# Optimization experiments

Measured on AMD Instinct MI355X. Metric: run time of the kernel, lower is better.

## Reference

```python
import jax, jax.numpy as jnp
import numpy as np

DEPTH = 4      # truncation depth of the signature
DIM = 8        # path channels
PATH_LEN = 16384
STREAM = True


def _restricted_exp(z, depth):
    # exp(z) in truncated tensor algebra: level k term = z^{\otimes k}/k!, flattened to [d**k]
    terms = [z]
    for k in range(2, depth + 1):
        terms.append((terms[-1][:, None] * z[None, :]).reshape(-1) / k)
    return tuple(terms)


def _chen_mult(a, b, depth):
    # Truncated tensor-algebra product (Chen's relation); a_0 = b_0 = 1 implicit.
    # c_k = a_k + b_k + sum_{i=1}^{k-1} a_i \otimes b_{k-i}
    c = []
    for k in range(depth):
        t = a[k] + b[k]
        for i in range(k):
            t = t + (a[i][:, None] * b[k - 1 - i][None, :]).reshape(-1)
        c.append(t)
    return tuple(c)


def setup_inputs() -> dict:
    key = jax.random.key(0)
    path = jax.random.normal(key, (PATH_LEN, DIM), dtype=jnp.float32)
    return {"path": path}


def reference(path):
    depth = DEPTH
    d = path.shape[-1]
    inc = path[1:] - path[:-1]                                # [N-1, d] increments
    exps = jax.vmap(lambda z: _restricted_exp(z, depth))(inc)  # tuple of [N-1, d**k]
    init = tuple(jnp.zeros((d ** (k + 1),), dtype=path.dtype) for k in range(depth))

    def step(carry, x):
        new = _chen_mult(carry, x, depth)
        return new, (new if STREAM else None)

    last, ys = jax.lax.scan(step, init, exps)
    if STREAM:
        # flatten: concat levels -> [N-1, d + d^2 + ... + d^depth]
        return jnp.concatenate([y for y in ys], axis=-1)
    return jnp.concatenate(last, axis=-1)
```

## Files before the change

kernel.cpp:

```cpp
#include <hip/hip_runtime.h>

#define NPATH 16384
#define DIM   8
#define NINC  (NPATH - 1)
#define SIG   4680
#define L1OFF 0
#define L2OFF 8
#define L3OFF 72
#define L4OFF 584
#define NCHUNK 256
#define CHUNK  64
#define NSUB  1024
#define SUB   16
#define SPC   4
#define NGRP  16
#define GSIZE 16
#define C6    0.16666666666666666f
#define LPAD  17


__device__ __forceinline__ void light_barrier() {
  asm volatile("s_waitcnt lgkmcnt(0)" ::: "memory");
  __builtin_amdgcn_s_barrier();
}

__device__ __forceinline__ void zero_state(float r4[16], float r3[2],
                                           float& a1i, float& a2v,
                                           float& a2s, float& a1s, float& a1t) {
#pragma unroll
  for (int l = 0; l < 16; ++l) r4[l] = 0.f;
  r3[0] = r3[1] = 0.f;
  a1i = a2v = a2s = a1s = a1t = 0.f;
}

__device__ __forceinline__ void store_sig_reg(float* __restrict__ dst,
                                              const float r4[16], const float r3[2],
                                              float a2s, float a1t, int t) {
  float4* d4 = (float4*)(dst + L4OFF + 16 * t);
  d4[0] = make_float4(r4[0], r4[1], r4[2], r4[3]);
  d4[1] = make_float4(r4[4], r4[5], r4[6], r4[7]);
  d4[2] = make_float4(r4[8], r4[9], r4[10], r4[11]);
  d4[3] = make_float4(r4[12], r4[13], r4[14], r4[15]);
  *(float2*)(dst + L3OFF + 2 * t) = make_float2(r3[0], r3[1]);
  if (t < 64) dst[L2OFF + t] = a2s;
  if (t < 8)  dst[L1OFF + t] = a1t;
}

__device__ __forceinline__ void load_state(const float* __restrict__ src,
                                           float r4[16], float r3[2],
                                           float& a1i, float& a2v,
                                           float& a2s, float& a1s, float& a1t, int t) {
  const float4* s4 = (const float4*)(src + L4OFF + 16 * t);
  float4 G0 = s4[0], G1 = s4[1], G2 = s4[2], G3 = s4[3];
  r4[0]=G0.x; r4[1]=G0.y; r4[2]=G0.z; r4[3]=G0.w;
  r4[4]=G1.x; r4[5]=G1.y; r4[6]=G1.z; r4[7]=G1.w;
  r4[8]=G2.x; r4[9]=G2.y; r4[10]=G2.z; r4[11]=G2.w;
  r4[12]=G3.x; r4[13]=G3.y; r4[14]=G3.z; r4[15]=G3.w;
  const float2 gr3 = *(const float2*)(src + L3OFF + 2 * t);
  r3[0] = gr3.x; r3[1] = gr3.y;
  a1i = src[L1OFF + (t >> 5)];
  a2v = src[L2OFF + (t >> 2)];
  a2s = a1s = a1t = 0.f;
  if (t < 64) { a2s = src[L2OFF + t]; a1s = src[L1OFF + (t >> 3)]; }
  if (t < 8)  { a1t = src[L1OFF + t]; }
}

__device__ __forceinline__ void chen_reg(float r4[16], float r3[2],
                                         float& a1i, float& a2v,
                                         float& a2s, float& a1s, float& a1t,
                                         const float* __restrict__ b, int t) {
  const int i   = t >> 5;
  const int j   = (t >> 2) & 7;
  const int ij  = t >> 2;
  const int c0  = 2 * t;
  const int jk0 = c0 & 63;
  const int k0  = 2 * (t & 3);
  const int i2  = t >> 3;
  const int j2  = t & 7;
  const float4* bv = (const float4*)b;
  float4 B0 = bv[146 + 4 * t], B1 = bv[147 + 4 * t], B2 = bv[148 + 4 * t], B3 = bv[149 + 4 * t];
  float4 Cq0 = bv[18 + 2 * jk0], Cq1 = bv[19 + 2 * jk0], Cq2 = bv[20 + 2 * jk0], Cq3 = bv[21 + 2 * jk0];
  float4 D0 = bv[2 + 2 * k0], D1 = bv[3 + 2 * k0], D2 = bv[4 + 2 * k0], D3 = bv[5 + 2 * k0];
  float4 E0 = bv[0], E1 = bv[1];
  const float2 b3c  = *(const float2*)(b + L3OFF + c0);
  const float2 b2jk = *(const float2*)(b + L2OFF + jk0);
  const float2 b1k  = *(const float2*)(b + L1OFF + k0);
  const float b2ij = b[L2OFF + ij];
  const float b1j  = b[L1OFF + j];
  const float b1i  = b[L1OFF + i];
  float b2t = 0.f, b1j2 = 0.f, b1i2 = 0.f, b1t = 0.f;
  if (t < 64) { b2t = b[L2OFF + t]; b1j2 = b[L1OFF + j2]; b1i2 = b[L1OFF + i2]; }
  if (t < 8)  { b1t = b[L1OFF + t]; }

  const float b4r[16] = {B0.x,B0.y,B0.z,B0.w, B1.x,B1.y,B1.z,B1.w,
                         B2.x,B2.y,B2.z,B2.w, B3.x,B3.y,B3.z,B3.w};
  const float b3r[16] = {Cq0.x,Cq0.y,Cq0.z,Cq0.w, Cq1.x,Cq1.y,Cq1.z,Cq1.w,
                         Cq2.x,Cq2.y,Cq2.z,Cq2.w, Cq3.x,Cq3.y,Cq3.z,Cq3.w};
  const float b2r[16] = {D0.x,D0.y,D0.z,D0.w, D1.x,D1.y,D1.z,D1.w,
                         D2.x,D2.y,D2.z,D2.w, D3.x,D3.y,D3.z,D3.w};
  const float b1r[8]  = {E0.x,E0.y,E0.z,E0.w, E1.x,E1.y,E1.z,E1.w};

#pragma unroll
  for (int l = 0; l < 8; ++l) {
    r4[l]     += b4r[l]     + a1i * b3r[l]     + a2v * b2r[l]     + r3[0] * b1r[l];
    r4[8 + l] += b4r[8 + l] + a1i * b3r[8 + l] + a2v * b2r[8 + l] + r3[1] * b1r[l];
  }
  r3[0] += b3c.x + a1i * b2jk.x + a2v * b1k.x;
  r3[1] += b3c.y + a1i * b2jk.y + a2v * b1k.y;
  const float a1i_old = a1i;
  a2v += b2ij + a1i_old * b1j;
  if (t < 64) { a2s += b2t + a1s * b1j2; a1s += b1i2; }
  a1i = a1i_old + b1i;
  if (t < 8) a1t += b1t;
}

struct ChenB {
  float4 B0, B1, B2, B3;
  float4 C0, C1, C2, C3;
  float4 D0, D1, D2, D3;
  float4 E0, E1;
  float2 b3c, b2jk, b1k;
  float  b2ij, b1j, b1i, b2t, b1j2, b1i2, b1t;
};

__device__ __forceinline__ void chen_load(const float* __restrict__ b, int t, ChenB& R) {
  const int i   = t >> 5;
  const int j   = (t >> 2) & 7;
  const int ij  = t >> 2;
  const int c0  = 2 * t;
  const int jk0 = c0 & 63;
  const int k0  = 2 * (t & 3);
  const int i2  = t >> 3;
  const int j2  = t & 7;
  const float4* bv = (const float4*)b;
  R.B0 = bv[146 + 4 * t]; R.B1 = bv[147 + 4 * t]; R.B2 = bv[148 + 4 * t]; R.B3 = bv[149 + 4 * t];
  R.C0 = bv[18 + 2 * jk0]; R.C1 = bv[19 + 2 * jk0]; R.C2 = bv[20 + 2 * jk0]; R.C3 = bv[21 + 2 * jk0];
  R.D0 = bv[2 + 2 * k0]; R.D1 = bv[3 + 2 * k0]; R.D2 = bv[4 + 2 * k0]; R.D3 = bv[5 + 2 * k0];
  R.E0 = bv[0]; R.E1 = bv[1];
  R.b3c  = *(const float2*)(b + L3OFF + c0);
  R.b2jk = *(const float2*)(b + L2OFF + jk0);
  R.b1k  = *(const float2*)(b + L1OFF + k0);
  R.b2ij = b[L2OFF + ij];
  R.b1j  = b[L1OFF + j];
  R.b1i  = b[L1OFF + i];
  R.b2t = 0.f; R.b1j2 = 0.f; R.b1i2 = 0.f; R.b1t = 0.f;
  if (t < 64) { R.b2t = b[L2OFF + t]; R.b1j2 = b[L1OFF + j2]; R.b1i2 = b[L1OFF + i2]; }
  if (t < 8)  { R.b1t = b[L1OFF + t]; }
}

__device__ __forceinline__ void chen_apply(float r4[16], float r3[2],
                                           float& a1i, float& a2v,
                                           float& a2s, float& a1s, float& a1t,
                                           const ChenB& R, int t) {
  const float b4r[16] = {R.B0.x,R.B0.y,R.B0.z,R.B0.w, R.B1.x,R.B1.y,R.B1.z,R.B1.w,
                         R.B2.x,R.B2.y,R.B2.z,R.B2.w, R.B3.x,R.B3.y,R.B3.z,R.B3.w};
  const float b3r[16] = {R.C0.x,R.C0.y,R.C0.z,R.C0.w, R.C1.x,R.C1.y,R.C1.z,R.C1.w,
                         R.C2.x,R.C2.y,R.C2.z,R.C2.w, R.C3.x,R.C3.y,R.C3.z,R.C3.w};
  const float b2r[16] = {R.D0.x,R.D0.y,R.D0.z,R.D0.w, R.D1.x,R.D1.y,R.D1.z,R.D1.w,
                         R.D2.x,R.D2.y,R.D2.z,R.D2.w, R.D3.x,R.D3.y,R.D3.z,R.D3.w};
  const float b1r[8]  = {R.E0.x,R.E0.y,R.E0.z,R.E0.w, R.E1.x,R.E1.y,R.E1.z,R.E1.w};
#pragma unroll
  for (int l = 0; l < 8; ++l) {
    r4[l]     += b4r[l]     + a1i * b3r[l]     + a2v * b2r[l]     + r3[0] * b1r[l];
    r4[8 + l] += b4r[8 + l] + a1i * b3r[8 + l] + a2v * b2r[8 + l] + r3[1] * b1r[l];
  }
  r3[0] += R.b3c.x + a1i * R.b2jk.x + a2v * R.b1k.x;
  r3[1] += R.b3c.y + a1i * R.b2jk.y + a2v * R.b1k.y;
  const float a1i_old = a1i;
  a2v += R.b2ij + a1i_old * R.b1j;
  if (t < 64) { a2s += R.b2t + a1s * R.b1j2; a1s += R.b1i2; }
  a1i = a1i_old + R.b1i;
  if (t < 8) a1t += R.b1t;
}

__device__ __forceinline__ void step_update(const float* zs,
                                            float r4[16], float r3[2],
                                            float& a1i, float& a2v,
                                            float& a2s, float& a1s, float& a1t, int t) {
  const int i  = t >> 5;
  const int j  = (t >> 2) & 7;
  const int k0 = 2 * (t & 3);
  const int i2 = t >> 3;
  const int j2 = t & 7;
  const float zi = zs[i];
  const float zj = zs[j];
  const float2 zk = *(const float2*)(zs + k0);
  const float4 za = *(const float4*)zs;
  const float4 zb = *(const float4*)(zs + 4);
  const float zn[8] = {za.x, za.y, za.z, za.w, zb.x, zb.y, zb.z, zb.w};
  const float a1zi4 = a1i + 0.25f * zi;
  const float zj6   = C6 * zj;
  const float T0 = r3[0] + a2v * (0.5f * zk.x) + a1zi4 * (zj6 * zk.x);
  const float T1 = r3[1] + a2v * (0.5f * zk.y) + a1zi4 * (zj6 * zk.y);
  const float U  = a2v + (0.5f * a1i + C6 * zi) * zj;
#pragma unroll
  for (int l = 0; l < 8; ++l) {
    r4[l]     += T0 * zn[l];
    r4[8 + l] += T1 * zn[l];
  }
  r3[0] += zk.x * U;
  r3[1] += zk.y * U;
  a2v += (a1i + 0.5f * zi) * zj;
  a1i += zi;
  if (t < 64) {
    const float zi2 = zs[i2], zj2v = zs[j2];
    a2s += (a1s + 0.5f * zi2) * zj2v;
    a1s += zi2;
  }
  if (t < 8) a1t += zs[t];
}

__global__ __launch_bounds__(256) void k_totals(const float* __restrict__ path,
                                                float* __restrict__ T64,
                                                float* __restrict__ snap) {
  __shared__ float zbuf[CHUNK][8];
  const int t = threadIdx.x;
  const int b = blockIdx.x;
  const int base = b * CHUNK;
  for (int u = t; u < CHUNK * 8; u += 256) {
    const int s = u >> 3, l = u & 7;
    const int rB = min(base + s + 1, NPATH - 1);
    zbuf[s][l] = path[rB * DIM + l] - path[(base + s) * DIM + l];
  }
  float r4[16], r3[2], a1i, a2v, a2s, a1s, a1t;
  zero_state(r4, r3, a1i, a2v, a2s, a1s, a1t);
  __syncthreads();
  for (int w = 0; w < SPC; ++w) {
    if (w > 0) store_sig_reg(snap + ((size_t)b * SPC + w) * SIG, r4, r3, a2s, a1t, t);
#pragma unroll
    for (int s2 = 0; s2 < SUB; ++s2)
      step_update(zbuf[SUB * w + s2], r4, r3, a1i, a2v, a2s, a1s, a1t, t);
  }
  store_sig_reg(T64 + (size_t)b * SIG, r4, r3, a2s, a1t, t);
}

__global__ __launch_bounds__(256) void k_scan(const float* __restrict__ in,
                                              float* __restrict__ prefout,
                                              float* __restrict__ totout,
                                              int count) {
  const int t = threadIdx.x;
  const size_t goff = (size_t)blockIdx.x * count;
  float r4[16], r3[2], a1i, a2v, a2s, a1s, a1t;
  zero_state(r4, r3, a1i, a2v, a2s, a1s, a1t);
  ChenB bA, bB;
  chen_load(in + goff * SIG, t, bA);
  for (int m = 0; m < count; m += 2) {
    if (m + 1 < count) chen_load(in + (goff + m + 1) * SIG, t, bB);
    store_sig_reg(prefout + (goff + m) * SIG, r4, r3, a2s, a1t, t);
    chen_apply(r4, r3, a1i, a2v, a2s, a1s, a1t, bA, t);
    if (m + 1 >= count) break;
    if (m + 2 < count) chen_load(in + (goff + m + 2) * SIG, t, bA);
    store_sig_reg(prefout + (goff + m + 1) * SIG, r4, r3, a2s, a1t, t);
    chen_apply(r4, r3, a1i, a2v, a2s, a1s, a1t, bB, t);
  }
  if (totout != nullptr) store_sig_reg(totout + (size_t)blockIdx.x * SIG, r4, r3, a2s, a1t, t);
}

__global__ __launch_bounds__(256) void k_out(const float* __restrict__ path,
                                             const float* __restrict__ pref,
                                             const float* __restrict__ gpref,
                                             const float* __restrict__ snap,
                                             float* __restrict__ out) {
  __shared__ float zbuf[SUB][8];
  __shared__ __align__(16) float lbuf[256 * LPAD];
  const int t = threadIdx.x;
  const int sIdx = blockIdx.x;
  const int b = sIdx >> 2;
  const int g = b >> 4;
  const int base = sIdx * SUB;
  const int n = min(SUB, NINC - base);
  for (int u = t; u < SUB * 8; u += 256) {
    const int s = u >> 3, l = u & 7;
    const int rB = min(base + s + 1, NPATH - 1);
    zbuf[s][l] = path[rB * DIM + l] - path[(base + s) * DIM + l];
  }
  float r4[16], r3[2], a1i, a2v, a2s, a1s, a1t;
  load_state(gpref + (size_t)g * SIG, r4, r3, a1i, a2v, a2s, a1s, a1t, t);
  chen_reg(r4, r3, a1i, a2v, a2s, a1s, a1t, pref + (size_t)b * SIG, t);
  if (sIdx & 3)
    chen_reg(r4, r3, a1i, a2v, a2s, a1s, a1t, snap + (size_t)sIdx * SIG, t);
  __syncthreads();
  const int tp = t >> 2;
  const int rq = 4 * (t & 3);
  for (int s2 = 0; s2 < n; ++s2) {
    step_update(zbuf[s2], r4, r3, a1i, a2v, a2s, a1s, a1t, t);
    float* lb = lbuf + LPAD * t;
    *(float4*)(lb + 0)  = make_float4(r4[0], r4[1], r4[2], r4[3]);
    *(float4*)(lb + 4)  = make_float4(r4[4], r4[5], r4[6], r4[7]);
    *(float4*)(lb + 8)  = make_float4(r4[8], r4[9], r4[10], r4[11]);
    *(float4*)(lb + 12) = make_float4(r4[12], r4[13], r4[14], r4[15]);
    light_barrier();
    float* dst = out + (size_t)(base + s2) * SIG;
#pragma unroll
    for (int q = 0; q < 4; ++q) {
      const float4 v = *(const float4*)(lbuf + LPAD * (tp + 64 * q) + rq);
      *(float4*)(dst + L4OFF + 4 * t + 1024 * q) = v;
    }
    *(float2*)(dst + L3OFF + 2 * t) = make_float2(r3[0], r3[1]);
    if (t < 64) dst[L2OFF + t] = a2s;
    if (t < 8)  dst[L1OFF + t] = a1t;
    light_barrier();
  }
}

extern "C" void kernel_launch(void* const* d_in, const int* in_sizes, int n_in,
                              void* d_out, int out_size, void* d_ws, size_t ws_size,
                              hipStream_t stream) {
  (void)in_sizes; (void)n_in; (void)out_size; (void)ws_size;
  const float* path = (const float*)d_in[0];
  float* out = (float*)d_out;
  float* ws = (float*)d_ws;

  float* T64    = ws;
  float* pref   = T64    + (size_t)NCHUNK * SIG;
  float* gtot   = pref   + (size_t)NCHUNK * SIG;
  float* gpref  = gtot   + (size_t)NGRP * SIG;
  float* snap   = gpref  + (size_t)NGRP * SIG;

  k_totals<<<NCHUNK, 256, 0, stream>>>(path, T64, snap);
  k_scan<<<NGRP, 256, 0, stream>>>(T64, pref, gtot, GSIZE);
  k_scan<<<1, 256, 0, stream>>>(gtot, gpref, nullptr, NGRP);
  k_out<<<NSUB, 256, 0, stream>>>(path, pref, gpref, snap, out);
}
```

Measured before the change: 139.1 us.

## Drop group-prefix scan kernel, fold group totals into output kernel, use nontemporal stores

Removes the single-block scan over group totals. Each output block now combines the preceding group totals itself with a serial loop of Chen products before applying the chunk prefix and snapshot. This saves one serial launch but makes later blocks do up to 16 extra Chen products. The change also adds nontemporal stores for the streamed output, a launch-bounds occupancy hint, and unroll 4 on the main step loop.

```diff
diff --git a/kernel.cpp b/kernel.cpp
--- a/kernel.cpp
+++ b/kernel.cpp
@@ -18,6 +18,8 @@
 #define C6    0.16666666666666666f
 #define LPAD  17
 
+typedef float vfloat4 __attribute__((ext_vector_type(4)));
+typedef float vfloat2 __attribute__((ext_vector_type(2)));
 
 __device__ __forceinline__ void light_barrier() {
   asm volatile("s_waitcnt lgkmcnt(0)" ::: "memory");
@@ -44,25 +46,6 @@
   *(float2*)(dst + L3OFF + 2 * t) = make_float2(r3[0], r3[1]);
   if (t < 64) dst[L2OFF + t] = a2s;
   if (t < 8)  dst[L1OFF + t] = a1t;
-}
-
-__device__ __forceinline__ void load_state(const float* __restrict__ src,
-                                           float r4[16], float r3[2],
-                                           float& a1i, float& a2v,
-                                           float& a2s, float& a1s, float& a1t, int t) {
-  const float4* s4 = (const float4*)(src + L4OFF + 16 * t);
-  float4 G0 = s4[0], G1 = s4[1], G2 = s4[2], G3 = s4[3];
-  r4[0]=G0.x; r4[1]=G0.y; r4[2]=G0.z; r4[3]=G0.w;
-  r4[4]=G1.x; r4[5]=G1.y; r4[6]=G1.z; r4[7]=G1.w;
-  r4[8]=G2.x; r4[9]=G2.y; r4[10]=G2.z; r4[11]=G2.w;
-  r4[12]=G3.x; r4[13]=G3.y; r4[14]=G3.z; r4[15]=G3.w;
-  const float2 gr3 = *(const float2*)(src + L3OFF + 2 * t);
-  r3[0] = gr3.x; r3[1] = gr3.y;
-  a1i = src[L1OFF + (t >> 5)];
-  a2v = src[L2OFF + (t >> 2)];
-  a2s = a1s = a1t = 0.f;
-  if (t < 64) { a2s = src[L2OFF + t]; a1s = src[L1OFF + (t >> 3)]; }
-  if (t < 8)  { a1t = src[L1OFF + t]; }
 }
 
 __device__ __forceinline__ void chen_reg(float r4[16], float r3[2],
@@ -256,11 +239,11 @@
   if (totout != nullptr) store_sig_reg(totout + (size_t)blockIdx.x * SIG, r4, r3, a2s, a1t, t);
 }
 
-__global__ __launch_bounds__(256) void k_out(const float* __restrict__ path,
-                                             const float* __restrict__ pref,
-                                             const float* __restrict__ gpref,
-                                             const float* __restrict__ snap,
-                                             float* __restrict__ out) {
+__global__ __launch_bounds__(256, 5) void k_out(const float* __restrict__ path,
+                                                const float* __restrict__ pref,
+                                                const float* __restrict__ GT,
+                                                const float* __restrict__ snap,
+                                                float* __restrict__ out) {
   __shared__ float zbuf[SUB][8];
   __shared__ __align__(16) float lbuf[256 * LPAD];
   const int t = threadIdx.x;
@@ -269,19 +252,24 @@
   const int g = b >> 4;
   const int base = sIdx * SUB;
   const int n = min(SUB, NINC - base);
-  for (int u = t; u < SUB * 8; u += 256) {
-    const int s = u >> 3, l = u & 7;
+  if (t < SUB * 8) {
+    const int s = t >> 3, l = t & 7;
     const int rB = min(base + s + 1, NPATH - 1);
     zbuf[s][l] = path[rB * DIM + l] - path[(base + s) * DIM + l];
   }
   float r4[16], r3[2], a1i, a2v, a2s, a1s, a1t;
-  load_state(gpref + (size_t)g * SIG, r4, r3, a1i, a2v, a2s, a1s, a1t, t);
-  chen_reg(r4, r3, a1i, a2v, a2s, a1s, a1t, pref + (size_t)b * SIG, t);
-  if (sIdx & 3)
-    chen_reg(r4, r3, a1i, a2v, a2s, a1s, a1t, snap + (size_t)sIdx * SIG, t);
+  zero_state(r4, r3, a1i, a2v, a2s, a1s, a1t);
+  const int cnt = g + 1 + ((sIdx & 3) ? 1 : 0);
+  for (int m = 0; m < cnt; ++m) {
+    const float* bp = (m < g) ? GT + (size_t)m * SIG
+                   : (m == g) ? pref + (size_t)b * SIG
+                              : snap + (size_t)sIdx * SIG;
+    chen_reg(r4, r3, a1i, a2v, a2s, a1s, a1t, bp, t);
+  }
   __syncthreads();
   const int tp = t >> 2;
   const int rq = 4 * (t & 3);
+#pragma unroll 4
   for (int s2 = 0; s2 < n; ++s2) {
     step_update(zbuf[s2], r4, r3, a1i, a2v, a2s, a1s, a1t, t);
     float* lb = lbuf + LPAD * t;
@@ -293,12 +281,13 @@
     float* dst = out + (size_t)(base + s2) * SIG;
 #pragma unroll
     for (int q = 0; q < 4; ++q) {
-      const float4 v = *(const float4*)(lbuf + LPAD * (tp + 64 * q) + rq);
-      *(float4*)(dst + L4OFF + 4 * t + 1024 * q) = v;
+      const vfloat4 v = *(const vfloat4*)(lbuf + LPAD * (tp + 64 * q) + rq);
+      __builtin_nontemporal_store(v, (vfloat4*)(dst + L4OFF + 4 * t + 1024 * q));
     }
-    *(float2*)(dst + L3OFF + 2 * t) = make_float2(r3[0], r3[1]);
-    if (t < 64) dst[L2OFF + t] = a2s;
-    if (t < 8)  dst[L1OFF + t] = a1t;
+    vfloat2 r3v; r3v.x = r3[0]; r3v.y = r3[1];
+    __builtin_nontemporal_store(r3v, (vfloat2*)(dst + L3OFF + 2 * t));
+    if (t < 64) __builtin_nontemporal_store(a2s, dst + L2OFF + t);
+    if (t < 8)  __builtin_nontemporal_store(a1t, dst + L1OFF + t);
     light_barrier();
   }
 }
@@ -313,12 +302,10 @@
 
   float* T64    = ws;
   float* pref   = T64    + (size_t)NCHUNK * SIG;
-  float* gtot   = pref   + (size_t)NCHUNK * SIG;
-  float* gpref  = gtot   + (size_t)NGRP * SIG;
-  float* snap   = gpref  + (size_t)NGRP * SIG;
+  float* GT     = pref   + (size_t)NCHUNK * SIG;
+  float* snap   = GT     + (size_t)NGRP * SIG;
 
   k_totals<<<NCHUNK, 256, 0, stream>>>(path, T64, snap);
-  k_scan<<<NGRP, 256, 0, stream>>>(T64, pref, gtot, GSIZE);
-  k_scan<<<1, 256, 0, stream>>>(gtot, gpref, nullptr, NGRP);
-  k_out<<<NSUB, 256, 0, stream>>>(path, pref, gpref, snap, out);
-}
+  k_scan<<<NGRP, 256, 0, stream>>>(T64, pref, GT, GSIZE);
+  k_out<<<NSUB, 256, 0, stream>>>(path, pref, GT, snap, out);
+}
```

New measurement: 137.3 us. No clear change (-1.3%).
